# Optimization experiments

Hardware: AMD Instinct MI355X
Metric: run time of the kernel (lower is better)

## Reference

```python
import jax, jax.numpy as jnp
import numpy as np

IN_FEATURES = 4096
OUT_FEATURES = 11008
BLOCK_SIZE = 256
BPR = IN_FEATURES // BLOCK_SIZE  # blocks per row = 16


def setup_inputs() -> dict:
    key = jax.random.key(0)
    k1, k2, k3, k4, k5 = jax.random.split(key, 5)
    x = jax.random.normal(k1, (2, 2048, IN_FEATURES), dtype=jnp.float32)
    indices = jax.random.randint(k2, (OUT_FEATURES, IN_FEATURES), 0, 256, dtype=jnp.int32)
    scales = jax.random.uniform(k3, (OUT_FEATURES * BPR,), dtype=jnp.float32)
    biases_ab = jax.random.normal(k4, (OUT_FEATURES * BPR,), dtype=jnp.float32) * 0.02
    bias = jax.random.normal(k5, (OUT_FEATURES,), dtype=jnp.float32)
    return {"x": x, "indices": indices, "scales": scales, "biases_ab": biases_ab, "bias": bias}


def _dequant(indices, scales, biases_ab):
    # W[i, j] = ((idx - 128) / 127) * scale[block] + bias_ab[block]
    q = (indices.astype(jnp.float32) - 128.0) / 127.0          # [O, I]
    q = q.reshape(OUT_FEATURES, BPR, BLOCK_SIZE)               # [O, bpr, bs]
    s = scales.reshape(OUT_FEATURES, BPR, 1)
    b = biases_ab.reshape(OUT_FEATURES, BPR, 1)
    return (q * s + b).reshape(OUT_FEATURES, IN_FEATURES)      # [O, I]


def reference(x, indices, scales, biases_ab, bias):
    W = _dequant(indices, scales, biases_ab)                   # [O, I]
    x2d = x.reshape(-1, IN_FEATURES)                           # [N, I]
    out = jnp.einsum('ni,oi->no', x2d, W) + bias[None, :]      # [N, O]
    return out.reshape(*x.shape[:-1], OUT_FEATURES)
```

## Files before the change

kernel.cpp:

```cpp
#include <hip/hip_runtime.h>

#define K_DIM 4096
#define O_DIM 11008
#define QBLK  256
#define BPR   (K_DIM / QBLK)

typedef _Float16 f16;
typedef _Float16 f16x8 __attribute__((ext_vector_type(8)));
typedef float    f32x4 __attribute__((ext_vector_type(4)));

__global__ __launch_bounds__(256) void cvt_x_kernel(const float* __restrict__ x,
                                                    f16* __restrict__ xh) {
    size_t i = ((size_t)blockIdx.x * 256 + threadIdx.x) * 8;
    float4 a = *(const float4*)(x + i);
    float4 b = *(const float4*)(x + i + 4);
    f16x8 h;
    h[0] = (f16)a.x; h[1] = (f16)a.y; h[2] = (f16)a.z; h[3] = (f16)a.w;
    h[4] = (f16)b.x; h[5] = (f16)b.y; h[6] = (f16)b.z; h[7] = (f16)b.w;
    *(f16x8*)(xh + i) = h;
}

__global__ __launch_bounds__(256) void dequant_w_kernel(const int* __restrict__ qidx,
                                                        const float* __restrict__ scales,
                                                        const float* __restrict__ babs,
                                                        f16* __restrict__ wh) {
    size_t e = ((size_t)blockIdx.x * 256 + threadIdx.x) * 8;
    int4 q0 = *(const int4*)(qidx + e);
    int4 q1 = *(const int4*)(qidx + e + 4);
    int sb = (int)(e >> 8);
    float s2 = scales[sb] * (1.0f / 127.0f);
    float b2 = fmaf(-128.0f, s2, babs[sb]);
    f16x8 h;
    h[0] = (f16)fmaf((float)q0.x, s2, b2);
    h[1] = (f16)fmaf((float)q0.y, s2, b2);
    h[2] = (f16)fmaf((float)q0.z, s2, b2);
    h[3] = (f16)fmaf((float)q0.w, s2, b2);
    h[4] = (f16)fmaf((float)q1.x, s2, b2);
    h[5] = (f16)fmaf((float)q1.y, s2, b2);
    h[6] = (f16)fmaf((float)q1.z, s2, b2);
    h[7] = (f16)fmaf((float)q1.w, s2, b2);
    *(f16x8*)(wh + e) = h;
}

#define BM 128
#define BN 128
#define BK 64
#define NBN (O_DIM / BN)

__global__ __launch_bounds__(256, 3) void gemm_f16_kernel(const f16* __restrict__ A,
                                                          const f16* __restrict__ B,
                                                          const float* __restrict__ bias,
                                                          float* __restrict__ out) {
    __shared__ f16 As[BM * BK];
    __shared__ f16 Bs[BN * BK];

    int bid = blockIdx.x;
    int chunk = gridDim.x >> 3;
    int swz = (bid & 7) * chunk + (bid >> 3);
    int bm = swz / NBN;
    int bn = swz - bm * NBN;

    const int tid  = threadIdx.x;
    const int lane = tid & 63;
    const int wid  = tid >> 6;
    const int wr   = wid >> 1;
    const int wc   = wid & 1;
    const int fr   = lane & 15;
    const int fq   = lane >> 4;

    const size_t arow0 = (size_t)bm * BM;
    const size_t brow0 = (size_t)bn * BN;
    const f16* ga = A + arow0 * K_DIM;
    const f16* gb = B + brow0 * K_DIM;

    f32x4 acc[4][4];
    #pragma unroll
    for (int m = 0; m < 4; ++m)
        #pragma unroll
        for (int n = 0; n < 4; ++n)
            acc[m][n] = (f32x4){0.f, 0.f, 0.f, 0.f};

    for (int kt = 0; kt < K_DIM / BK; ++kt) {
        const int k0 = kt * BK;
        #pragma unroll
        for (int c = 0; c < 4; ++c) {
            int bo  = (c * 256 + tid) * 16;
            int row = bo >> 7;
            int col = (bo & 127) >> 1;
            __builtin_amdgcn_global_load_lds(
                (const __attribute__((address_space(1))) void*)(ga + (size_t)row * K_DIM + k0 + col),
                (__attribute__((address_space(3))) void*)(As + (bo >> 1)),
                16, 0, 0);
            __builtin_amdgcn_global_load_lds(
                (const __attribute__((address_space(1))) void*)(gb + (size_t)row * K_DIM + k0 + col),
                (__attribute__((address_space(3))) void*)(Bs + (bo >> 1)),
                16, 0, 0);
        }
        __syncthreads();

        #pragma unroll
        for (int kk = 0; kk < 2; ++kk) {
            f16x8 af[4], bf[4];
            #pragma unroll
            for (int m = 0; m < 4; ++m)
                af[m] = *(const f16x8*)(As + (wr * 64 + m * 16 + fr) * BK + kk * 32 + fq * 8);
            #pragma unroll
            for (int n = 0; n < 4; ++n)
                bf[n] = *(const f16x8*)(Bs + (wc * 64 + n * 16 + fr) * BK + kk * 32 + fq * 8);
            #pragma unroll
            for (int m = 0; m < 4; ++m)
                #pragma unroll
                for (int n = 0; n < 4; ++n)
                    acc[m][n] = __builtin_amdgcn_mfma_f32_16x16x32_f16(af[m], bf[n], acc[m][n], 0, 0, 0);
        }
        __syncthreads();
    }

    #pragma unroll
    for (int m = 0; m < 4; ++m) {
        int grow = (int)arow0 + wr * 64 + m * 16 + fq * 4;
        #pragma unroll
        for (int n = 0; n < 4; ++n) {
            int gcol = (int)brow0 + wc * 64 + n * 16 + fr;
            float bv = bias[gcol];
            #pragma unroll
            for (int r = 0; r < 4; ++r)
                out[(size_t)(grow + r) * O_DIM + gcol] = acc[m][n][r] + bv;
        }
    }
}

__global__ __launch_bounds__(256) void fallback_kernel(const float* __restrict__ x,
                                                       const int* __restrict__ qidx,
                                                       const float* __restrict__ scales,
                                                       const float* __restrict__ babs,
                                                       const float* __restrict__ bias,
                                                       float* __restrict__ out) {
    __shared__ float xs[K_DIM];
    int n = blockIdx.x;
    int o = blockIdx.y * 256 + threadIdx.x;
    for (int i = threadIdx.x; i < K_DIM; i += 256)
        xs[i] = x[(size_t)n * K_DIM + i];
    __syncthreads();
    const int* qr = qidx + (size_t)o * K_DIM;
    float sum = 0.f;
    for (int b = 0; b < BPR; ++b) {
        float s2 = scales[o * BPR + b] * (1.0f / 127.0f);
        float b2 = fmaf(-128.0f, s2, babs[o * BPR + b]);
        for (int k = 0; k < QBLK; ++k)
            sum = fmaf(xs[b * QBLK + k], fmaf((float)qr[b * QBLK + k], s2, b2), sum);
    }
    out[(size_t)n * O_DIM + o] = sum + bias[o];
}

extern "C" void kernel_launch(void* const* d_in, const int* in_sizes, int n_in,
                              void* d_out, int out_size, void* d_ws, size_t ws_size,
                              hipStream_t stream) {
    const float* x      = (const float*)d_in[0];
    const int*   qidx   = (const int*)d_in[1];
    const float* scales = (const float*)d_in[2];
    const float* babs   = (const float*)d_in[3];
    const float* bias   = (const float*)d_in[4];
    float* out = (float*)d_out;

    const int nrows = in_sizes[0] / K_DIM;

    const size_t xh_bytes = (size_t)nrows * K_DIM * sizeof(f16);
    const size_t wh_bytes = (size_t)O_DIM * K_DIM * sizeof(f16);

    if (ws_size >= xh_bytes + wh_bytes) {
        f16* xh = (f16*)d_ws;
        f16* wh = (f16*)((char*)d_ws + xh_bytes);

        int cvt_blocks = (int)(((size_t)nrows * K_DIM) / 2048);
        cvt_x_kernel<<<cvt_blocks, 256, 0, stream>>>(x, xh);

        int dq_blocks = (int)(((size_t)O_DIM * K_DIM) / 2048);
        dequant_w_kernel<<<dq_blocks, 256, 0, stream>>>(qidx, scales, babs, wh);

        int nwg = (nrows / BM) * NBN;
        gemm_f16_kernel<<<nwg, 256, 0, stream>>>(xh, wh, bias, out);
    } else {
        dim3 grid(nrows, O_DIM / 256);
        fallback_kernel<<<grid, 256, 0, stream>>>(x, qidx, scales, babs, bias, out);
    }
}
```

Measured before the change: 768.2 us.

## Use 256x256 GEMM tiles with 4-stage async LDS pipeline and swizzled layout

Replaces the 128x128x64 GEMM with a 512-thread 256x256x32 tile kernel. Each wave now computes a 128x64 output sub-tile, which raises data reuse per LDS read. Global-to-LDS loads run three stages ahead in a 4-buffer ring, synchronised with explicit vmcnt waits and raw barriers instead of the load-then-syncthreads pattern. An XOR swizzle on LDS slots avoids bank conflicts, and setprio raises priority around the MFMA block. The cost is 128KB of LDS per block and high accumulator register pressure, so occupancy is limited to one block per CU.

```diff
diff --git a/kernel.cpp b/kernel.cpp
--- a/kernel.cpp
+++ b/kernel.cpp
@@ -42,17 +42,18 @@
     *(f16x8*)(wh + e) = h;
 }
 
-#define BM 128
-#define BN 128
-#define BK 64
+#define BM 256
+#define BN 256
+#define BK 32
+#define NT (K_DIM / BK)
 #define NBN (O_DIM / BN)
-
-__global__ __launch_bounds__(256, 3) void gemm_f16_kernel(const f16* __restrict__ A,
-                                                          const f16* __restrict__ B,
-                                                          const float* __restrict__ bias,
-                                                          float* __restrict__ out) {
-    __shared__ f16 As[BM * BK];
-    __shared__ f16 Bs[BN * BK];
+#define TILE_E (BM * BK)
+
+__global__ __launch_bounds__(512, 2) void gemm256_f16_kernel(const f16* __restrict__ A,
+                                                             const f16* __restrict__ B,
+                                                             const float* __restrict__ bias,
+                                                             float* __restrict__ out) {
+    __shared__ f16 smem[4][2][TILE_E];
 
     int bid = blockIdx.x;
     int chunk = gridDim.x >> 3;
@@ -63,65 +64,103 @@
     const int tid  = threadIdx.x;
     const int lane = tid & 63;
     const int wid  = tid >> 6;
-    const int wr   = wid >> 1;
-    const int wc   = wid & 1;
+    const int wr   = wid >> 2;
+    const int wc   = wid & 3;
     const int fr   = lane & 15;
     const int fq   = lane >> 4;
 
-    const size_t arow0 = (size_t)bm * BM;
-    const size_t brow0 = (size_t)bn * BN;
-    const f16* ga = A + arow0 * K_DIM;
-    const f16* gb = B + brow0 * K_DIM;
-
-    f32x4 acc[4][4];
-    #pragma unroll
-    for (int m = 0; m < 4; ++m)
+    const f16* gA = A + (size_t)bm * BM * K_DIM;
+    const f16* gB = B + (size_t)bn * BN * K_DIM;
+
+    const int srow  = tid >> 2;
+    const int sslot = (tid & 3) ^ ((tid >> 3) & 3);
+    const size_t goff = (size_t)srow * K_DIM + sslot * 8;
+    const int loff = tid * 8;
+
+    int aoffs[8], boffs[4];
+    #pragma unroll
+    for (int m = 0; m < 8; ++m) {
+        int r = wr * 128 + m * 16 + fr;
+        aoffs[m] = r * BK + ((fq ^ ((r >> 1) & 3)) << 3);
+    }
+    #pragma unroll
+    for (int n = 0; n < 4; ++n) {
+        int r = wc * 64 + n * 16 + fr;
+        boffs[n] = r * BK + ((fq ^ ((r >> 1) & 3)) << 3);
+    }
+
+    f32x4 acc[8][4];
+    #pragma unroll
+    for (int m = 0; m < 8; ++m)
         #pragma unroll
         for (int n = 0; n < 4; ++n)
             acc[m][n] = (f32x4){0.f, 0.f, 0.f, 0.f};
 
-    for (int kt = 0; kt < K_DIM / BK; ++kt) {
-        const int k0 = kt * BK;
-        #pragma unroll
-        for (int c = 0; c < 4; ++c) {
-            int bo  = (c * 256 + tid) * 16;
-            int row = bo >> 7;
-            int col = (bo & 127) >> 1;
-            __builtin_amdgcn_global_load_lds(
-                (const __attribute__((address_space(1))) void*)(ga + (size_t)row * K_DIM + k0 + col),
-                (__attribute__((address_space(3))) void*)(As + (bo >> 1)),
-                16, 0, 0);
-            __builtin_amdgcn_global_load_lds(
-                (const __attribute__((address_space(1))) void*)(gb + (size_t)row * K_DIM + k0 + col),
-                (__attribute__((address_space(3))) void*)(Bs + (bo >> 1)),
-                16, 0, 0);
+#define STAGE(tt)                                                                        \
+    do {                                                                                 \
+        int _b = (tt) & 3;                                                               \
+        size_t _k = (size_t)(tt) * BK;                                                   \
+        __builtin_amdgcn_global_load_lds(                                                \
+            (const __attribute__((address_space(1))) void*)(gA + _k + goff),             \
+            (__attribute__((address_space(3))) void*)(&smem[_b][0][loff]), 16, 0, 0);    \
+        __builtin_amdgcn_global_load_lds(                                                \
+            (const __attribute__((address_space(1))) void*)(gA + _k + goff + (size_t)128 * K_DIM), \
+            (__attribute__((address_space(3))) void*)(&smem[_b][0][loff + 4096]), 16, 0, 0); \
+        __builtin_amdgcn_global_load_lds(                                                \
+            (const __attribute__((address_space(1))) void*)(gB + _k + goff),             \
+            (__attribute__((address_space(3))) void*)(&smem[_b][1][loff]), 16, 0, 0);    \
+        __builtin_amdgcn_global_load_lds(                                                \
+            (const __attribute__((address_space(1))) void*)(gB + _k + goff + (size_t)128 * K_DIM), \
+            (__attribute__((address_space(3))) void*)(&smem[_b][1][loff + 4096]), 16, 0, 0); \
+    } while (0)
+
+    STAGE(0);
+    STAGE(1);
+    STAGE(2);
+
+    for (int t = 0; t < NT; ++t) {
+        __builtin_amdgcn_s_barrier();
+
+        if (t < NT - 3) {
+            STAGE(t + 3);
+            asm volatile("s_waitcnt vmcnt(12)" ::: "memory");
+        } else if (t == NT - 3) {
+            asm volatile("s_waitcnt vmcnt(8)" ::: "memory");
+        } else if (t == NT - 2) {
+            asm volatile("s_waitcnt vmcnt(4)" ::: "memory");
+        } else {
+            asm volatile("s_waitcnt vmcnt(0)" ::: "memory");
         }
-        __syncthreads();
-
-        #pragma unroll
-        for (int kk = 0; kk < 2; ++kk) {
-            f16x8 af[4], bf[4];
-            #pragma unroll
-            for (int m = 0; m < 4; ++m)
-                af[m] = *(const f16x8*)(As + (wr * 64 + m * 16 + fr) * BK + kk * 32 + fq * 8);
+
+        __builtin_amdgcn_s_barrier();
+
+        const f16* Asb = &smem[t & 3][0][0];
+        const f16* Bsb = &smem[t & 3][1][0];
+
+        f16x8 af[8], bf[4];
+        #pragma unroll
+        for (int m = 0; m < 8; ++m)
+            af[m] = *(const f16x8*)(Asb + aoffs[m]);
+        #pragma unroll
+        for (int n = 0; n < 4; ++n)
+            bf[n] = *(const f16x8*)(Bsb + boffs[n]);
+
+        __builtin_amdgcn_s_setprio(1);
+        #pragma unroll
+        for (int m = 0; m < 8; ++m)
             #pragma unroll
             for (int n = 0; n < 4; ++n)
-                bf[n] = *(const f16x8*)(Bs + (wc * 64 + n * 16 + fr) * BK + kk * 32 + fq * 8);
-            #pragma unroll
-            for (int m = 0; m < 4; ++m)
-                #pragma unroll
-                for (int n = 0; n < 4; ++n)
-                    acc[m][n] = __builtin_amdgcn_mfma_f32_16x16x32_f16(af[m], bf[n], acc[m][n], 0, 0, 0);
-        }
-        __syncthreads();
-    }
-
-    #pragma unroll
-    for (int m = 0; m < 4; ++m) {
-        int grow = (int)arow0 + wr * 64 + m * 16 + fq * 4;
+                acc[m][n] = __builtin_amdgcn_mfma_f32_16x16x32_f16(af[m], bf[n], acc[m][n], 0, 0, 0);
+        __builtin_amdgcn_s_setprio(0);
+    }
+#undef STAGE
+
+    #pragma unroll
+    for (int m = 0; m < 8; ++m) {
+        int grow = bm * BM + wr * 128 + m * 16 + fq * 4;
         #pragma unroll
         for (int n = 0; n < 4; ++n) {
-            int gcol = (int)brow0 + wc * 64 + n * 16 + fr;
+            int gcol = bn * BN + wc * 64 + n * 16 + fr;
             float bv = bias[gcol];
             #pragma unroll
             for (int r = 0; r < 4; ++r)
@@ -168,7 +207,7 @@
     const size_t xh_bytes = (size_t)nrows * K_DIM * sizeof(f16);
     const size_t wh_bytes = (size_t)O_DIM * K_DIM * sizeof(f16);
 
-    if (ws_size >= xh_bytes + wh_bytes) {
+    if (ws_size >= xh_bytes + wh_bytes && (nrows % BM) == 0) {
         f16* xh = (f16*)d_ws;
         f16* wh = (f16*)((char*)d_ws + xh_bytes);
 
@@ -179,7 +218,7 @@
         dequant_w_kernel<<<dq_blocks, 256, 0, stream>>>(qidx, scales, babs, wh);
 
         int nwg = (nrows / BM) * NBN;
-        gemm_f16_kernel<<<nwg, 256, 0, stream>>>(xh, wh, bias, out);
+        gemm256_f16_kernel<<<nwg, 512, 0, stream>>>(xh, wh, bias, out);
     } else {
         dim3 grid(nrows, O_DIM / 256);
         fallback_kernel<<<grid, 256, 0, stream>>>(x, qidx, scales, babs, bias, out);
```

After: 727.2 us. -5.3%, faster.
